# Kernel optimization log

Hardware: AMD Instinct MI355X
Metric: run time of the kernel (lower is better)

## Reference

```python
import jax, jax.numpy as jnp
import numpy as np

N_AGENT = 25
N_S = 32
N_A = 4
HID = 128
EHH_HID = HID * N_AGENT          # 3200
INTER = 150                      # INTERMEDIATE_NODES
BATCH = 2048
N_EDGE = 300


def _leaky(x):
    return jnp.where(x >= 0, x, 0.01 * x)


def setup_inputs() -> dict:
    key = jax.random.key(0)
    ks = jax.random.split(key, 12)
    states = jax.random.normal(ks[0], (N_AGENT, BATCH, N_S), dtype=jnp.float32)
    ehh_w = jax.random.normal(ks[1], (N_AGENT * N_S, EHH_HID), dtype=jnp.float32) * 0.05
    anova = jax.random.normal(ks[2], (EHH_HID + INTER, N_AGENT), dtype=jnp.float32)
    w1 = jax.random.normal(ks[3], (N_AGENT, EHH_HID, 12), dtype=jnp.float32) * 0.02
    b1 = jax.random.normal(ks[4], (N_AGENT, 12), dtype=jnp.float32) * 0.02
    w2 = jax.random.normal(ks[5], (N_AGENT, 12, 12), dtype=jnp.float32) * 0.3
    b2 = jax.random.normal(ks[6], (N_AGENT, 12), dtype=jnp.float32) * 0.02
    w3 = jax.random.normal(ks[7], (N_AGENT, 12, N_A), dtype=jnp.float32) * 0.3
    b3 = jax.random.normal(ks[8], (N_AGENT, N_A), dtype=jnp.float32) * 0.02
    actions = jax.random.randint(ks[9], (N_AGENT, BATCH), 0, N_A, dtype=jnp.int32)
    # adjacency rows: (bi_att_row, neighbor_row_a, unused, neighbor_row_b)
    c0 = jax.random.randint(ks[10], (N_EDGE, 1), 0, INTER, dtype=jnp.int32)
    c13 = jax.random.randint(ks[11], (N_EDGE, 2), 0, EHH_HID, dtype=jnp.int32)
    adj = jnp.concatenate([c0, c13[:, :1], jnp.zeros((N_EDGE, 1), jnp.int32), c13[:, 1:]], axis=1)
    return {"states": states, "ehh_w": ehh_w, "anova": anova,
            "w1": w1, "b1": b1, "w2": w2, "b2": b2, "w3": w3, "b3": b3,
            "actions": actions, "adj": adj}


def reference(states, ehh_w, anova, w1, b1, w2, b2, w3, b3, actions, adj):
    # states: (A, B, S) -> ehh_s: (B, A*S)   (torch.cat(states, dim=1))
    B = states.shape[1]
    ehh_s = jnp.transpose(states, (1, 0, 2)).reshape(B, -1)
    # EHH normalization (BatchNorm, affine=False, batch stats) + linear + LeakyReLU
    mu = jnp.mean(ehh_s, axis=0, keepdims=True)
    var = jnp.var(ehh_s, axis=0, keepdims=True)
    ehh_n = (ehh_s - mu) * jax.lax.rsqrt(var + 1e-5)
    ehh_embedding = _leaky(ehh_n @ ehh_w)                    # (B, EHH_HID)

    # ANOVA attention assembly via adjacency scatter
    self_att = anova[:EHH_HID, :]                            # (EHH_HID, A)
    bi_att = anova[EHH_HID:, :]                              # (INTER, A)
    vals = bi_att[adj[:, 0], :]                              # (E, A)
    neighbor_att = jnp.zeros((EHH_HID, N_AGENT), jnp.float32)
    neighbor_att = neighbor_att.at[adj[:, 1]].set(vals)
    neighbor_att = neighbor_att.at[adj[:, 3]].set(vals)
    all_att = (self_att + neighbor_att).T                    # (A, EHH_HID)

    # att_s repeat/permute/reshape == broadcast of embedding per agent
    att_out = ehh_embedding[:, None, :] * all_att[None, :, :]  # (B, A, EHH_HID)

    # per-agent critics (ehh_hidden -> 12 -> 12 -> n_a)
    h1 = _leaky(jnp.einsum('bah,ahk->bak', att_out, w1) + b1[None])
    h2 = _leaky(jnp.einsum('bak,akj->baj', h1, w2) + b2[None])
    all_q = jnp.einsum('baj,ajc->bac', h2, w3) + b3[None]     # (B, A, N_A)

    # q = all_q.gather(1, in_acs) per agent -> (A, B)
    q = jnp.take_along_axis(all_q, actions.T[:, :, None], axis=2)[..., 0].T
    return q
```

## Files before the change

kernel.cpp:

```cpp
#include <hip/hip_runtime.h>
#include <cstdint>

#define NAG 25
#define NS 32
#define EHH 3200
#define KDIM 800
#define BATCH 2048
#define NEDGE 300
#define NPAD 384
#define KSPLIT 4

typedef _Float16 half8 __attribute__((ext_vector_type(8)));
typedef float f32x4 __attribute__((ext_vector_type(4)));

__device__ __forceinline__ float leaky(float x) { return x >= 0.f ? x : 0.01f * x; }

__global__ void init_kernel(float* __restrict__ acc, int* __restrict__ winner) {
    int t = blockIdx.x * 256 + threadIdx.x;
    if (t < 1600) acc[t] = 0.f;
    if (t < EHH) winner[t] = -1;
}

__global__ void stats_part(const float* __restrict__ states, float* __restrict__ acc) {
    int a = blockIdx.x;
    int chunk = blockIdx.y;
    int s = threadIdx.x & 31, ty = threadIdx.x >> 5;
    const float* base = states + ((size_t)a * BATCH + chunk * 128) * NS + s;
    float sum = 0.f, sq = 0.f;
    for (int b = ty; b < 128; b += 8) {
        float v = base[(size_t)b * NS];
        sum += v; sq += v * v;
    }
    __shared__ float ls[8][32], lq[8][32];
    ls[ty][s] = sum; lq[ty][s] = sq;
    __syncthreads();
    if (ty == 0) {
#pragma unroll
        for (int i = 1; i < 8; ++i) { sum += ls[i][s]; sq += lq[i][s]; }
        atomicAdd(&acc[a * 32 + s], sum);
        atomicAdd(&acc[800 + a * 32 + s], sq);
    }
}

__global__ void norma_kernel(const float* __restrict__ states, const float* __restrict__ acc,
                             _Float16* __restrict__ A) {
    int t = blockIdx.x * 256 + threadIdx.x;
    int b = t / KDIM;
    int f = t - b * KDIM;
    int a = f >> 5, s = f & 31;
    float m = acc[f] * (1.f / BATCH);
    float var = acc[800 + f] * (1.f / BATCH) - m * m;
    float rs = rsqrtf(var + 1e-5f);
    float v = states[((size_t)a * BATCH + b) * NS + s];
    A[t] = (_Float16)((v - m) * rs);
}

__global__ void wtrans_kernel(const float* __restrict__ w, _Float16* __restrict__ wt) {
    __shared__ float tile[32][33];
    int n0 = blockIdx.x * 32, k0 = blockIdx.y * 32;
    int x = threadIdx.x, y = threadIdx.y;
    for (int i = y; i < 32; i += 8)
        tile[i][x] = w[(size_t)(k0 + i) * EHH + n0 + x];
    __syncthreads();
    for (int i = y; i < 32; i += 8)
        wt[(size_t)(n0 + i) * KDIM + k0 + x] = (_Float16)tile[x][i];
}

__global__ void scatter_win(const int* __restrict__ adj, int* __restrict__ winner) {
    int e = blockIdx.x * 256 + threadIdx.x;
    if (e < 2 * NEDGE) {
        int pass = e >= NEDGE;
        int ee = pass ? e - NEDGE : e;
        int dest = adj[ee * 4 + (pass ? 3 : 1)];
        atomicMax(&winner[dest], e);
    }
}

__global__ void w2d_kernel(const float* __restrict__ anova, const int* __restrict__ adj,
                           const int* __restrict__ winner, const float* __restrict__ w1,
                           _Float16* __restrict__ w2dt) {
    int h = blockIdx.x * 128 + threadIdx.x;
    int n = blockIdx.y;
    float v = 0.f;
    if (n < 300) {
        int a = n / 12, kk = n - a * 12;
        float att = anova[(size_t)h * NAG + a];
        int w = winner[h];
        if (w >= 0) {
            int ee = w >= NEDGE ? w - NEDGE : w;
            int src = adj[ee * 4 + 0];
            att += anova[(size_t)(EHH + src) * NAG + a];
        }
        v = att * w1[((size_t)a * EHH + h) * 12 + kk];
    }
    w2dt[(size_t)n * EHH + h] = (_Float16)v;
}

__device__ __forceinline__ void async16(const void* g, void* l) {
    __builtin_amdgcn_global_load_lds(
        (const __attribute__((address_space(1))) void*)(uintptr_t)g,
        (__attribute__((address_space(3))) void*)(unsigned)(uintptr_t)l, 16, 0, 0);
}

template <bool LEAKY_F16_OUT>
__global__ __launch_bounds__(256)
void gemm_bt(const _Float16* __restrict__ A, const _Float16* __restrict__ B,
             _Float16* __restrict__ Ch, float* __restrict__ Cf,
             int Ktot, int ldc, int kPerSplit, int slabStride) {
    __shared__ __attribute__((aligned(16))) _Float16 As[128 * 32];
    __shared__ __attribute__((aligned(16))) _Float16 Bs[128 * 32];
    const int tid = threadIdx.x;
    const int lane = tid & 63;
    const int wave = tid >> 6;
    const int wm = (wave >> 1) << 6;
    const int wn = (wave & 1) << 6;
    const int m0 = blockIdx.x << 7;
    const int n0 = blockIdx.y << 7;
    const int k0 = blockIdx.z * kPerSplit;
    const int nk = kPerSplit >> 5;

    const int srow = lane >> 2;
    const int scol = (lane & 3) << 3;
    const _Float16* gA0 = A + (size_t)(m0 + wave * 16 + srow) * Ktot + k0 + scol;
    const _Float16* gA1 = gA0 + (size_t)64 * Ktot;
    const _Float16* gB0 = B + (size_t)(n0 + wave * 16 + srow) * Ktot + k0 + scol;
    const _Float16* gB1 = gB0 + (size_t)64 * Ktot;
    _Float16* lA0 = As + wave * 512;
    _Float16* lA1 = As + 2048 + wave * 512;
    _Float16* lB0 = Bs + wave * 512;
    _Float16* lB1 = Bs + 2048 + wave * 512;

    f32x4 acc[4][4];
    const f32x4 zero = {0.f, 0.f, 0.f, 0.f};
#pragma unroll
    for (int i = 0; i < 4; ++i)
#pragma unroll
        for (int j = 0; j < 4; ++j) acc[i][j] = zero;

    const int fr = lane & 15;
    const int q8 = (lane >> 4) << 3;

    for (int kt = 0; kt < nk; ++kt) {
        const int ko = kt << 5;
        __syncthreads();
        async16(gA0 + ko, lA0);
        async16(gA1 + ko, lA1);
        async16(gB0 + ko, lB0);
        async16(gB1 + ko, lB1);
        __syncthreads();

        half8 av[4], bv[4];
#pragma unroll
        for (int i = 0; i < 4; ++i)
            av[i] = *(const half8*)(As + (wm + i * 16 + fr) * 32 + q8);
#pragma unroll
        for (int j = 0; j < 4; ++j)
            bv[j] = *(const half8*)(Bs + (wn + j * 16 + fr) * 32 + q8);
#pragma unroll
        for (int i = 0; i < 4; ++i)
#pragma unroll
            for (int j = 0; j < 4; ++j)
                acc[i][j] = __builtin_amdgcn_mfma_f32_16x16x32_f16(av[i], bv[j], acc[i][j], 0, 0, 0);
    }

    const int r0 = (lane >> 4) << 2;
    if (LEAKY_F16_OUT) {
#pragma unroll
        for (int i = 0; i < 4; ++i)
#pragma unroll
            for (int j = 0; j < 4; ++j)
#pragma unroll
                for (int r = 0; r < 4; ++r) {
                    int row = m0 + wm + i * 16 + r0 + r;
                    int col = n0 + wn + j * 16 + fr;
                    Ch[(size_t)row * ldc + col] = (_Float16)leaky(acc[i][j][r]);
                }
    } else {
        float* C = Cf + (size_t)blockIdx.z * slabStride;
#pragma unroll
        for (int i = 0; i < 4; ++i)
#pragma unroll
            for (int j = 0; j < 4; ++j)
#pragma unroll
                for (int r = 0; r < 4; ++r) {
                    int row = m0 + wm + i * 16 + r0 + r;
                    int col = n0 + wn + j * 16 + fr;
                    C[(size_t)row * ldc + col] = acc[i][j][r];
                }
    }
}

__global__ void tail_kernel(const float* __restrict__ Hp, const float* __restrict__ b1,
                            const float* __restrict__ w2, const float* __restrict__ b2,
                            const float* __restrict__ w3, const float* __restrict__ b3,
                            const int* __restrict__ act, float* __restrict__ out) {
    int t = blockIdx.x * 256 + threadIdx.x;
    int b = t & (BATCH - 1);
    int a = t >> 11;
    const float* hp = Hp + (size_t)b * NPAD + a * 12;
    float h1[12];
#pragma unroll
    for (int k = 0; k < 12; ++k) {
        float s = b1[a * 12 + k];
#pragma unroll
        for (int ks = 0; ks < KSPLIT; ++ks) s += hp[(size_t)ks * BATCH * NPAD + k];
        h1[k] = leaky(s);
    }
    float h2[12];
#pragma unroll
    for (int j = 0; j < 12; ++j) {
        float s = b2[a * 12 + j];
#pragma unroll
        for (int k = 0; k < 12; ++k) s += h1[k] * w2[(a * 12 + k) * 12 + j];
        h2[j] = leaky(s);
    }
    int c = act[t];
    float q = b3[a * 4 + c];
#pragma unroll
    for (int j = 0; j < 12; ++j) q += h2[j] * w3[(a * 12 + j) * 4 + c];
    out[t] = q;
}

extern "C" void kernel_launch(void* const* d_in, const int* in_sizes, int n_in,
                              void* d_out, int out_size, void* d_ws, size_t ws_size,
                              hipStream_t stream) {
    (void)in_sizes; (void)n_in; (void)out_size; (void)ws_size;
    const float* states = (const float*)d_in[0];
    const float* ehh_w  = (const float*)d_in[1];
    const float* anova  = (const float*)d_in[2];
    const float* w1     = (const float*)d_in[3];
    const float* b1     = (const float*)d_in[4];
    const float* w2     = (const float*)d_in[5];
    const float* b2     = (const float*)d_in[6];
    const float* w3     = (const float*)d_in[7];
    const float* b3     = (const float*)d_in[8];
    const int* actions  = (const int*)d_in[9];
    const int* adj      = (const int*)d_in[10];
    float* out = (float*)d_out;

    char* ws = (char*)d_ws;
    float*     acc    = (float*)    (ws + 0);
    int*       winner = (int*)      (ws + 8192);
    _Float16*  Abf    = (_Float16*) (ws + 32768);
    _Float16*  WbT    = (_Float16*) (ws + 3311616);
    _Float16*  W2dT   = (_Float16*) (ws + 8433664);
    _Float16*  emb    = (_Float16*) (ws + 10893312);
    float*     Hp     = (float*)    (ws + 24002560);

    init_kernel<<<13, 256, 0, stream>>>(acc, winner);
    stats_part<<<dim3(25, 16), 256, 0, stream>>>(states, acc);
    norma_kernel<<<(BATCH * KDIM) / 256, 256, 0, stream>>>(states, acc, Abf);
    wtrans_kernel<<<dim3(EHH / 32, KDIM / 32), dim3(32, 8), 0, stream>>>(ehh_w, WbT);
    scatter_win<<<3, 256, 0, stream>>>(adj, winner);
    w2d_kernel<<<dim3(EHH / 128, NPAD), 128, 0, stream>>>(anova, adj, winner, w1, W2dT);
    gemm_bt<true><<<dim3(16, 25, 1), 256, 0, stream>>>(Abf, WbT, emb, nullptr, KDIM, EHH, KDIM, 0);
    gemm_bt<false><<<dim3(16, 3, KSPLIT), 256, 0, stream>>>(emb, W2dT, nullptr, Hp, EHH, NPAD,
                                                            EHH / KSPLIT, BATCH * NPAD);
    tail_kernel<<<(BATCH * NAG) / 256, 256, 0, stream>>>(Hp, b1, w2, b2, w3, b3, actions, out);
}
```

Before: 165.1 us.

## Double-buffer GEMM LDS tiles, fuse prep kernels, rework W2d build, raise K-split

```diff
diff --git a/kernel.cpp b/kernel.cpp
--- a/kernel.cpp
+++ b/kernel.cpp
@@ -8,7 +8,7 @@
 #define BATCH 2048
 #define NEDGE 300
 #define NPAD 384
-#define KSPLIT 4
+#define KSPLIT 5
 
 typedef _Float16 half8 __attribute__((ext_vector_type(8)));
 typedef float f32x4 __attribute__((ext_vector_type(4)));
@@ -42,58 +42,68 @@
     }
 }
 
-__global__ void norma_kernel(const float* __restrict__ states, const float* __restrict__ acc,
-                             _Float16* __restrict__ A) {
-    int t = blockIdx.x * 256 + threadIdx.x;
-    int b = t / KDIM;
-    int f = t - b * KDIM;
-    int a = f >> 5, s = f & 31;
-    float m = acc[f] * (1.f / BATCH);
-    float var = acc[800 + f] * (1.f / BATCH) - m * m;
-    float rs = rsqrtf(var + 1e-5f);
-    float v = states[((size_t)a * BATCH + b) * NS + s];
-    A[t] = (_Float16)((v - m) * rs);
-}
-
-__global__ void wtrans_kernel(const float* __restrict__ w, _Float16* __restrict__ wt) {
+__global__ void prep_kernel(const float* __restrict__ states, const float* __restrict__ acc,
+                            const float* __restrict__ ehh_w, const int* __restrict__ adj,
+                            int* __restrict__ winner,
+                            _Float16* __restrict__ A, _Float16* __restrict__ wt) {
     __shared__ float tile[32][33];
-    int n0 = blockIdx.x * 32, k0 = blockIdx.y * 32;
-    int x = threadIdx.x, y = threadIdx.y;
-    for (int i = y; i < 32; i += 8)
-        tile[i][x] = w[(size_t)(k0 + i) * EHH + n0 + x];
-    __syncthreads();
-    for (int i = y; i < 32; i += 8)
-        wt[(size_t)(n0 + i) * KDIM + k0 + x] = (_Float16)tile[x][i];
-}
-
-__global__ void scatter_win(const int* __restrict__ adj, int* __restrict__ winner) {
-    int e = blockIdx.x * 256 + threadIdx.x;
-    if (e < 2 * NEDGE) {
-        int pass = e >= NEDGE;
-        int ee = pass ? e - NEDGE : e;
-        int dest = adj[ee * 4 + (pass ? 3 : 1)];
-        atomicMax(&winner[dest], e);
+    int bi = blockIdx.x;
+    if (bi < 6400) {
+        int t = bi * 256 + threadIdx.x;
+        int b = t / KDIM;
+        int f = t - b * KDIM;
+        int a = f >> 5, s = f & 31;
+        float m = acc[f] * (1.f / BATCH);
+        float var = acc[800 + f] * (1.f / BATCH) - m * m;
+        float rs = rsqrtf(var + 1e-5f);
+        float v = states[((size_t)a * BATCH + b) * NS + s];
+        A[t] = (_Float16)((v - m) * rs);
+    } else if (bi < 8900) {
+        int bb = bi - 6400;
+        int n0 = (bb % 100) * 32, k0 = (bb / 100) * 32;
+        int x = threadIdx.x & 31, y = threadIdx.x >> 5;
+        for (int i = y; i < 32; i += 8)
+            tile[i][x] = ehh_w[(size_t)(k0 + i) * EHH + n0 + x];
+        __syncthreads();
+        for (int i = y; i < 32; i += 8)
+            wt[(size_t)(n0 + i) * KDIM + k0 + x] = (_Float16)tile[x][i];
+    } else {
+        int e = (bi - 8900) * 256 + threadIdx.x;
+        if (e < 2 * NEDGE) {
+            int pass = e >= NEDGE;
+            int ee = pass ? e - NEDGE : e;
+            int dest = adj[ee * 4 + (pass ? 3 : 1)];
+            atomicMax(&winner[dest], e);
+        }
     }
 }
 
 __global__ void w2d_kernel(const float* __restrict__ anova, const int* __restrict__ adj,
                            const int* __restrict__ winner, const float* __restrict__ w1,
                            _Float16* __restrict__ w2dt) {
-    int h = blockIdx.x * 128 + threadIdx.x;
-    int n = blockIdx.y;
-    float v = 0.f;
-    if (n < 300) {
-        int a = n / 12, kk = n - a * 12;
-        float att = anova[(size_t)h * NAG + a];
-        int w = winner[h];
-        if (w >= 0) {
-            int ee = w >= NEDGE ? w - NEDGE : w;
-            int src = adj[ee * 4 + 0];
-            att += anova[(size_t)(EHH + src) * NAG + a];
-        }
-        v = att * w1[((size_t)a * EHH + h) * 12 + kk];
-    }
-    w2dt[(size_t)n * EHH + h] = (_Float16)v;
+    if (blockIdx.x < 313) {
+        int t = blockIdx.x * 256 + threadIdx.x;
+        if (t < NAG * EHH) {
+            int a = t / EHH;
+            int h = t - a * EHH;
+            float att = anova[(size_t)h * NAG + a];
+            int w = winner[h];
+            if (w >= 0) {
+                int ee = w >= NEDGE ? w - NEDGE : w;
+                att += anova[(size_t)(EHH + adj[ee * 4]) * NAG + a];
+            }
+            const float* wp = w1 + ((size_t)a * EHH + h) * 12;
+#pragma unroll
+            for (int kk = 0; kk < 12; ++kk)
+                w2dt[(size_t)(a * 12 + kk) * EHH + h] = (_Float16)(att * wp[kk]);
+        }
+    } else {
+        int p = (blockIdx.x - 313) * 256 + threadIdx.x;
+        if (p < (NPAD - 300) * EHH / 8) {
+            half8 z = {0, 0, 0, 0, 0, 0, 0, 0};
+            ((half8*)(w2dt + (size_t)300 * EHH))[p] = z;
+        }
+    }
 }
 
 __device__ __forceinline__ void async16(const void* g, void* l) {
@@ -107,8 +117,8 @@
 void gemm_bt(const _Float16* __restrict__ A, const _Float16* __restrict__ B,
              _Float16* __restrict__ Ch, float* __restrict__ Cf,
              int Ktot, int ldc, int kPerSplit, int slabStride) {
-    __shared__ __attribute__((aligned(16))) _Float16 As[128 * 32];
-    __shared__ __attribute__((aligned(16))) _Float16 Bs[128 * 32];
+    __shared__ __attribute__((aligned(16))) _Float16 As[2][128 * 32];
+    __shared__ __attribute__((aligned(16))) _Float16 Bs[2][128 * 32];
     const int tid = threadIdx.x;
     const int lane = tid & 63;
     const int wave = tid >> 6;
@@ -125,10 +135,7 @@
     const _Float16* gA1 = gA0 + (size_t)64 * Ktot;
     const _Float16* gB0 = B + (size_t)(n0 + wave * 16 + srow) * Ktot + k0 + scol;
     const _Float16* gB1 = gB0 + (size_t)64 * Ktot;
-    _Float16* lA0 = As + wave * 512;
-    _Float16* lA1 = As + 2048 + wave * 512;
-    _Float16* lB0 = Bs + wave * 512;
-    _Float16* lB1 = Bs + 2048 + wave * 512;
+    const int lofs = wave * 512;
 
     f32x4 acc[4][4];
     const f32x4 zero = {0.f, 0.f, 0.f, 0.f};
@@ -140,22 +147,29 @@
     const int fr = lane & 15;
     const int q8 = (lane >> 4) << 3;
 
+    async16(gA0, As[0] + lofs);
+    async16(gA1, As[0] + 2048 + lofs);
+    async16(gB0, Bs[0] + lofs);
+    async16(gB1, Bs[0] + 2048 + lofs);
+
     for (int kt = 0; kt < nk; ++kt) {
-        const int ko = kt << 5;
+        const int cur = kt & 1;
         __syncthreads();
-        async16(gA0 + ko, lA0);
-        async16(gA1 + ko, lA1);
-        async16(gB0 + ko, lB0);
-        async16(gB1 + ko, lB1);
-        __syncthreads();
-
+        if (kt + 1 < nk) {
+            const int ko = (kt + 1) << 5;
+            const int nxt = cur ^ 1;
+            async16(gA0 + ko, As[nxt] + lofs);
+            async16(gA1 + ko, As[nxt] + 2048 + lofs);
+            async16(gB0 + ko, Bs[nxt] + lofs);
+            async16(gB1 + ko, Bs[nxt] + 2048 + lofs);
+        }
         half8 av[4], bv[4];
 #pragma unroll
         for (int i = 0; i < 4; ++i)
-            av[i] = *(const half8*)(As + (wm + i * 16 + fr) * 32 + q8);
+            av[i] = *(const half8*)(As[cur] + (wm + i * 16 + fr) * 32 + q8);
 #pragma unroll
         for (int j = 0; j < 4; ++j)
-            bv[j] = *(const half8*)(Bs + (wn + j * 16 + fr) * 32 + q8);
+            bv[j] = *(const half8*)(Bs[cur] + (wn + j * 16 + fr) * 32 + q8);
 #pragma unroll
         for (int i = 0; i < 4; ++i)
 #pragma unroll
@@ -249,10 +263,8 @@
 
     init_kernel<<<13, 256, 0, stream>>>(acc, winner);
     stats_part<<<dim3(25, 16), 256, 0, stream>>>(states, acc);
-    norma_kernel<<<(BATCH * KDIM) / 256, 256, 0, stream>>>(states, acc, Abf);
-    wtrans_kernel<<<dim3(EHH / 32, KDIM / 32), dim3(32, 8), 0, stream>>>(ehh_w, WbT);
-    scatter_win<<<3, 256, 0, stream>>>(adj, winner);
-    w2d_kernel<<<dim3(EHH / 128, NPAD), 128, 0, stream>>>(anova, adj, winner, w1, W2dT);
+    prep_kernel<<<8903, 256, 0, stream>>>(states, acc, ehh_w, adj, winner, Abf, WbT);
+    w2d_kernel<<<445, 256, 0, stream>>>(anova, adj, winner, w1, W2dT);
     gemm_bt<true><<<dim3(16, 25, 1), 256, 0, stream>>>(Abf, WbT, emb, nullptr, KDIM, EHH, KDIM, 0);
     gemm_bt<false><<<dim3(16, 3, KSPLIT), 256, 0, stream>>>(emb, W2dT, nullptr, Hp, EHH, NPAD,
                                                             EHH / KSPLIT, BATCH * NPAD);
```

Result: faster. 143.9 us (-12.8%).
